# Kernel optimization log

Hardware: AMD Instinct MI355X
Metric: run time of the kernel (lower is better)

## Reference

```python
import jax, jax.numpy as jnp
import numpy as np

N, D, H, E = 50000, 64, 8, 800000
NEG_SLOPE = 0.2


def setup_inputs() -> dict:
    key = jax.random.key(0)
    k1, k2, k3 = jax.random.split(key, 3)
    h_t = jax.random.normal(k1, (N, D), dtype=jnp.float32)
    edge_index = jax.random.randint(k2, (2, E), 0, N, dtype=jnp.int64)
    # xavier-uniform-like init for att [H, 2D]
    limit = float(np.sqrt(6.0 / (H + 2 * D)))
    att = jax.random.uniform(k3, (H, 2 * D), dtype=jnp.float32, minval=-limit, maxval=limit)
    return {"h_t": h_t, "edge_index": edge_index, "att": att}


def reference(h_t, edge_index, att):
    src, dst = edge_index[0], edge_index[1]
    # att[:, :D] multiplies h_i (dst features), att[:, D:] multiplies h_j (src features)
    # einsum('ehd,hd->eh', cat([h_i, h_j]), att) == (h_t @ att_dst.T)[dst] + (h_t @ att_src.T)[src]
    s_dst = h_t @ att[:, :D].T   # [N, H]
    s_src = h_t @ att[:, D:].T   # [N, H]
    e = s_dst[dst] + s_src[src]  # [E, H]
    e = jnp.where(e >= 0, e, NEG_SLOPE * e)  # leaky_relu
    # segment softmax over dst groups (numerically stable)
    e_max = jax.ops.segment_max(e, dst, num_segments=N)          # [N, H]
    ex = jnp.exp(e - e_max[dst])                                  # [E, H]
    denom = jax.ops.segment_sum(ex, dst, num_segments=N)         # [N, H]
    alpha = ex / denom[dst]                                       # [E, H]
    # weighted messages and scatter-add aggregate
    m = h_t[src][:, None, :] * alpha[:, :, None]                  # [E, H, D]
    out = jax.ops.segment_sum(m, dst, num_segments=N)             # [N, H, D]
    out = jnp.where(out > 0, out, jnp.expm1(out))                 # elu
    return out.reshape(N, H * D)
```

## Files before the change

### kernel.cpp

```cpp
#include <hip/hip_runtime.h>
#include <math.h>

#define NN 50000
#define DD 64
#define HH 8
#define EE 800000
#define NEG_SLOPE 0.2f
#define WPB 4
#define SCAN_B 1024
#define NB1 ((NN + SCAN_B - 1) / SCAN_B)

__global__ __launch_bounds__(256) void scores_kernel(
    const float* __restrict__ h_t, const float* __restrict__ att,
    float* __restrict__ s_dst, float* __restrict__ s_src) {
  __shared__ float hs[32 * 66];
  __shared__ float att_s[8 * 130];
  int tid = threadIdx.x;
  int node0 = blockIdx.x * 32;
  for (int q = tid; q < HH * 2 * DD; q += 256) {
    int h = q >> 7, k = q & 127;
    att_s[h * 130 + k] = att[q];
  }
  for (int q = tid; q < 32 * DD; q += 256) {
    int nl = q >> 6, d = q & 63;
    hs[nl * 66 + d] = (node0 + nl < NN) ? h_t[(size_t)(node0 + nl) * DD + d] : 0.0f;
  }
  __syncthreads();
  int nl = tid >> 3, h = tid & 7;
  int n = node0 + nl;
  float accd = 0.f, accs = 0.f;
#pragma unroll
  for (int d = 0; d < DD; ++d) {
    float hv = hs[nl * 66 + d];
    accd += hv * att_s[h * 130 + d];
    accs += hv * att_s[h * 130 + DD + d];
  }
  if (n < NN) {
    s_dst[n * HH + h] = accd;
    s_src[n * HH + h] = accs;
  }
}

__global__ __launch_bounds__(256) void count_kernel(const int* __restrict__ ei,
                                                    int* __restrict__ counts,
                                                    int* __restrict__ rank) {
  int t = blockIdx.x * 256 + threadIdx.x;
  if (t >= EE / 4) return;
  int4 v = ((const int4*)(ei + EE))[t];
  int4 r;
  r.x = atomicAdd(&counts[v.x], 1);
  r.y = atomicAdd(&counts[v.y], 1);
  r.z = atomicAdd(&counts[v.z], 1);
  r.w = atomicAdd(&counts[v.w], 1);
  ((int4*)rank)[t] = r;
}

__global__ __launch_bounds__(256) void scan1_kernel(const int* __restrict__ counts,
                                                    int* __restrict__ bsum) {
  int t = threadIdx.x;
  int base = blockIdx.x * SCAN_B + t * 4;
  int s = 0;
  if (base + 3 < NN) {
    int4 v = *(const int4*)(counts + base);
    s = v.x + v.y + v.z + v.w;
  } else {
    for (int k = 0; k < 4; ++k)
      if (base + k < NN) s += counts[base + k];
  }
#pragma unroll
  for (int m = 1; m < 64; m <<= 1) s += __shfl_xor(s, m);
  __shared__ int wsum[4];
  if ((t & 63) == 0) wsum[t >> 6] = s;
  __syncthreads();
  if (t == 0) bsum[blockIdx.x] = wsum[0] + wsum[1] + wsum[2] + wsum[3];
}

__global__ void scan2_kernel(const int* __restrict__ bsum, int* __restrict__ boff,
                             int* __restrict__ row_start) {
  int lane = threadIdx.x;
  int v = (lane < NB1) ? bsum[lane] : 0;
  int incl = v;
#pragma unroll
  for (int off = 1; off < 64; off <<= 1) {
    int u = __shfl_up(incl, off);
    if (lane >= off) incl += u;
  }
  if (lane < NB1) boff[lane] = incl - v;
  if (lane == 0) row_start[NN] = EE;
}

__global__ __launch_bounds__(256) void scan3_kernel(const int* __restrict__ counts,
                                                    const int* __restrict__ boff,
                                                    int* __restrict__ row_start) {
  int t = threadIdx.x, lane = t & 63, w = t >> 6;
  int base = blockIdx.x * SCAN_B + t * 4;
  int c[4] = {0, 0, 0, 0};
  bool full = (base + 3 < NN);
  if (full) {
    int4 v = *(const int4*)(counts + base);
    c[0] = v.x; c[1] = v.y; c[2] = v.z; c[3] = v.w;
  } else {
    for (int k = 0; k < 4; ++k)
      if (base + k < NN) c[k] = counts[base + k];
  }
  int tot = c[0] + c[1] + c[2] + c[3];
  int incl = tot;
#pragma unroll
  for (int off = 1; off < 64; off <<= 1) {
    int u = __shfl_up(incl, off);
    if (lane >= off) incl += u;
  }
  __shared__ int wt[4];
  if (lane == 63) wt[w] = incl;
  __syncthreads();
  int wpre = 0;
  for (int q = 0; q < w; ++q) wpre += wt[q];
  int p = boff[blockIdx.x] + wpre + incl - tot;
  int o0 = p, o1 = p + c[0], o2 = o1 + c[1], o3 = o2 + c[2];
  if (full) {
    *(int4*)(row_start + base) = make_int4(o0, o1, o2, o3);
  } else {
    int o[4] = {o0, o1, o2, o3};
    for (int k = 0; k < 4; ++k)
      if (base + k < NN) row_start[base + k] = o[k];
  }
}

__global__ __launch_bounds__(256) void fill_kernel(
    const int* __restrict__ ei, const int* __restrict__ row_start,
    const int* __restrict__ rank, int* __restrict__ sorted_src) {
  int t = blockIdx.x * 256 + threadIdx.x;
  if (t >= EE / 4) return;
  int4 s = ((const int4*)ei)[t];
  int4 d = ((const int4*)(ei + EE))[t];
  int4 r = ((const int4*)rank)[t];
  sorted_src[row_start[d.x] + r.x] = s.x;
  sorted_src[row_start[d.y] + r.y] = s.y;
  sorted_src[row_start[d.z] + r.z] = s.z;
  sorted_src[row_start[d.w] + r.w] = s.w;
}

__global__ __launch_bounds__(256) void fused_kernel(
    const float* __restrict__ h_t, const float* __restrict__ s_dst,
    const float* __restrict__ s_src, const int* __restrict__ row_start,
    const int* __restrict__ sorted_src, float* __restrict__ out) {
  __shared__ float p_lds[WPB][64][8];
  __shared__ int src_lds[WPB][64];
  int w = threadIdx.x >> 6, lane = threadIdx.x & 63;
  int n = blockIdx.x * WPB + w;
  if (n >= NN) return;
  float (*pw)[8] = p_lds[w];
  int* sw = src_lds[w];
  int beg = row_start[n], end = row_start[n + 1];
  int deg = end - beg;
  size_t ob = (size_t)n * 512 + lane;
  if (deg == 0) {
#pragma unroll
    for (int h = 0; h < 8; ++h) out[ob + h * 64] = 0.f;
    return;
  }
  int i = lane >> 3, hh = lane & 7;
  float sd = s_dst[n * 8 + hh];
  float m = -INFINITY, sum = 0.f;
  float acc[8];
#pragma unroll
  for (int h = 0; h < 8; ++h) acc[h] = 0.f;

  if (deg <= 64) {
    float v[8];
    int sreg[8];
#pragma unroll
    for (int k = 0; k < 8; ++k) {
      int e = i + 8 * k;
      if (e < deg) {
        int s = sorted_src[beg + e];
        sreg[k] = s;
        float x = sd + s_src[s * 8 + hh];
        x = x >= 0.f ? x : NEG_SLOPE * x;
        v[k] = x;
        m = fmaxf(m, x);
      }
    }
#pragma unroll
    for (int msk = 8; msk < 64; msk <<= 1) m = fmaxf(m, __shfl_xor(m, msk));
#pragma unroll
    for (int k = 0; k < 8; ++k) {
      int e = i + 8 * k;
      if (e < deg) {
        float p = __expf(v[k] - m);
        sum += p;
        pw[e][hh] = p;
        if (hh == 0) sw[e] = sreg[k];
      }
    }
#pragma unroll
    for (int msk = 8; msk < 64; msk <<= 1) sum += __shfl_xor(sum, msk);
    __builtin_amdgcn_wave_barrier();
    for (int e = 0; e < deg; ++e) {
      int s = sw[e];
      float hv = h_t[(size_t)s * 64 + lane];
      float4 pa = *(const float4*)&pw[e][0];
      float4 pb = *(const float4*)&pw[e][4];
      acc[0] = fmaf(hv, pa.x, acc[0]);
      acc[1] = fmaf(hv, pa.y, acc[1]);
      acc[2] = fmaf(hv, pa.z, acc[2]);
      acc[3] = fmaf(hv, pa.w, acc[3]);
      acc[4] = fmaf(hv, pb.x, acc[4]);
      acc[5] = fmaf(hv, pb.y, acc[5]);
      acc[6] = fmaf(hv, pb.z, acc[6]);
      acc[7] = fmaf(hv, pb.w, acc[7]);
    }
  } else {
    for (int c = 0; c < deg; c += 64) {
      int cnt = min(64, deg - c);
#pragma unroll
      for (int k = 0; k < 8; ++k) {
        int le = i + 8 * k;
        if (le < cnt) {
          int s = sorted_src[beg + c + le];
          float x = sd + s_src[s * 8 + hh];
          x = x >= 0.f ? x : NEG_SLOPE * x;
          m = fmaxf(m, x);
        }
      }
    }
#pragma unroll
    for (int msk = 8; msk < 64; msk <<= 1) m = fmaxf(m, __shfl_xor(m, msk));
    for (int c = 0; c < deg; c += 64) {
      int cnt = min(64, deg - c);
      __builtin_amdgcn_wave_barrier();
#pragma unroll
      for (int k = 0; k < 8; ++k) {
        int le = i + 8 * k;
        if (le < cnt) {
          int s = sorted_src[beg + c + le];
          float x = sd + s_src[s * 8 + hh];
          x = x >= 0.f ? x : NEG_SLOPE * x;
          float p = __expf(x - m);
          sum += p;
          pw[le][hh] = p;
          if (hh == 0) sw[le] = s;
        }
      }
      __builtin_amdgcn_wave_barrier();
      for (int e = 0; e < cnt; ++e) {
        int s = sw[e];
        float hv = h_t[(size_t)s * 64 + lane];
        float4 pa = *(const float4*)&pw[e][0];
        float4 pb = *(const float4*)&pw[e][4];
        acc[0] = fmaf(hv, pa.x, acc[0]);
        acc[1] = fmaf(hv, pa.y, acc[1]);
        acc[2] = fmaf(hv, pa.z, acc[2]);
        acc[3] = fmaf(hv, pa.w, acc[3]);
        acc[4] = fmaf(hv, pb.x, acc[4]);
        acc[5] = fmaf(hv, pb.y, acc[5]);
        acc[6] = fmaf(hv, pb.z, acc[6]);
        acc[7] = fmaf(hv, pb.w, acc[7]);
      }
    }
#pragma unroll
    for (int msk = 8; msk < 64; msk <<= 1) sum += __shfl_xor(sum, msk);
  }
  float rdv = 1.0f / sum;
#pragma unroll
  for (int h = 0; h < 8; ++h) {
    float rd = __shfl(rdv, h);
    float r = acc[h] * rd;
    r = r > 0.f ? r : expm1f(r);
    out[ob + h * 64] = r;
  }
}

extern "C" void kernel_launch(void* const* d_in, const int* in_sizes, int n_in,
                              void* d_out, int out_size, void* d_ws, size_t ws_size,
                              hipStream_t stream) {
  const float* h_t = (const float*)d_in[0];
  const int* ei = (const int*)d_in[1];
  const float* att = (const float*)d_in[2];
  float* out = (float*)d_out;

  char* ws = (char*)d_ws;
  size_t off = 0;
  auto alloc = [&](size_t bytes) {
    size_t cur = off;
    off += (bytes + 255) & ~(size_t)255;
    return cur;
  };
  float* s_dst = (float*)(ws + alloc((size_t)NN * HH * 4));
  float* s_src = (float*)(ws + alloc((size_t)NN * HH * 4));
  size_t zero_off = off;
  int* counts = (int*)(ws + alloc((size_t)NN * 4));
  size_t zero_bytes = off - zero_off;
  int* row_start = (int*)(ws + alloc((size_t)(NN + 1) * 4));
  int* sorted_src = (int*)(ws + alloc((size_t)EE * 4));
  int* rank = (int*)(ws + alloc((size_t)EE * 4));
  int* bsum = (int*)(ws + alloc((size_t)NB1 * 4));
  int* boff = (int*)(ws + alloc((size_t)NB1 * 4));

  hipMemsetAsync(ws + zero_off, 0, zero_bytes, stream);
  scores_kernel<<<(NN + 31) / 32, 256, 0, stream>>>(h_t, att, s_dst, s_src);
  count_kernel<<<(EE / 4 + 255) / 256, 256, 0, stream>>>(ei, counts, rank);
  scan1_kernel<<<NB1, 256, 0, stream>>>(counts, bsum);
  scan2_kernel<<<1, 64, 0, stream>>>(bsum, boff, row_start);
  scan3_kernel<<<NB1, 256, 0, stream>>>(counts, boff, row_start);
  fill_kernel<<<(EE / 4 + 255) / 256, 256, 0, stream>>>(ei, row_start, rank,
                                                        sorted_src);
  fused_kernel<<<NN / WPB, 256, 0, stream>>>(h_t, s_dst, s_src, row_start,
                                             sorted_src, out);
}
```

Baseline: 262.2 us.

## Gather bf16 node features in fused aggregation and merge scores with count kernel

Writes a bf16 copy of h_t inside the score kernel and has the aggregation loop gather 2 bf16 features per lane, with each half-wave handling alternate edges, then combines the halves by shuffle. This halves the gather bytes per edge and lets the final store be float2-wide. The separate score and count kernels become one launch split by block index, and the two degree branches are unified into one chunked loop. bf16 rounding of messages adds precision error against the fp32 reference.

```diff
diff --git a/kernel.cpp b/kernel.cpp
--- a/kernel.cpp
+++ b/kernel.cpp
@@ -9,21 +9,54 @@
 #define WPB 4
 #define SCAN_B 1024
 #define NB1 ((NN + SCAN_B - 1) / SCAN_B)
-
-__global__ __launch_bounds__(256) void scores_kernel(
+#define NB_SC ((NN + 31) / 32)
+#define NB_CT ((EE / 4 + 255) / 256)
+
+#define FMA16(H0, H1, PA, PB)                                              \
+  acc[0] = fmaf(H0, PA.x, acc[0]);   acc[1] = fmaf(H1, PA.x, acc[1]);      \
+  acc[2] = fmaf(H0, PA.y, acc[2]);   acc[3] = fmaf(H1, PA.y, acc[3]);      \
+  acc[4] = fmaf(H0, PA.z, acc[4]);   acc[5] = fmaf(H1, PA.z, acc[5]);      \
+  acc[6] = fmaf(H0, PA.w, acc[6]);   acc[7] = fmaf(H1, PA.w, acc[7]);      \
+  acc[8] = fmaf(H0, PB.x, acc[8]);   acc[9] = fmaf(H1, PB.x, acc[9]);      \
+  acc[10] = fmaf(H0, PB.y, acc[10]); acc[11] = fmaf(H1, PB.y, acc[11]);    \
+  acc[12] = fmaf(H0, PB.z, acc[12]); acc[13] = fmaf(H1, PB.z, acc[13]);    \
+  acc[14] = fmaf(H0, PB.w, acc[14]); acc[15] = fmaf(H1, PB.w, acc[15]);
+
+__global__ __launch_bounds__(256) void combo_kernel(
     const float* __restrict__ h_t, const float* __restrict__ att,
-    float* __restrict__ s_dst, float* __restrict__ s_src) {
+    const int* __restrict__ ei, float* __restrict__ s_dst,
+    float* __restrict__ s_src, unsigned short* __restrict__ h_bf,
+    int* __restrict__ counts, int* __restrict__ rank) {
+  if (blockIdx.x >= NB_SC) {
+    int t = (blockIdx.x - NB_SC) * 256 + threadIdx.x;
+    if (t >= EE / 4) return;
+    int4 v = ((const int4*)(ei + EE))[t];
+    int4 r;
+    r.x = atomicAdd(&counts[v.x], 1);
+    r.y = atomicAdd(&counts[v.y], 1);
+    r.z = atomicAdd(&counts[v.z], 1);
+    r.w = atomicAdd(&counts[v.w], 1);
+    ((int4*)rank)[t] = r;
+    return;
+  }
   __shared__ float hs[32 * 66];
   __shared__ float att_s[8 * 130];
   int tid = threadIdx.x;
   int node0 = blockIdx.x * 32;
   for (int q = tid; q < HH * 2 * DD; q += 256) {
-    int h = q >> 7, k = q & 127;
-    att_s[h * 130 + k] = att[q];
+    att_s[(q >> 7) * 130 + (q & 127)] = att[q];
   }
   for (int q = tid; q < 32 * DD; q += 256) {
     int nl = q >> 6, d = q & 63;
-    hs[nl * 66 + d] = (node0 + nl < NN) ? h_t[(size_t)(node0 + nl) * DD + d] : 0.0f;
+    int nd = node0 + nl;
+    float val = 0.f;
+    if (nd < NN) {
+      val = h_t[(size_t)nd * 64 + d];
+      unsigned u = __float_as_uint(val);
+      unsigned r = (u + 0x7fffu + ((u >> 16) & 1u)) >> 16;
+      h_bf[(size_t)nd * 64 + d] = (unsigned short)r;
+    }
+    hs[nl * 66 + d] = val;
   }
   __syncthreads();
   int nl = tid >> 3, h = tid & 7;
@@ -36,23 +69,9 @@
     accs += hv * att_s[h * 130 + DD + d];
   }
   if (n < NN) {
-    s_dst[n * HH + h] = accd;
-    s_src[n * HH + h] = accs;
-  }
-}
-
-__global__ __launch_bounds__(256) void count_kernel(const int* __restrict__ ei,
-                                                    int* __restrict__ counts,
-                                                    int* __restrict__ rank) {
-  int t = blockIdx.x * 256 + threadIdx.x;
-  if (t >= EE / 4) return;
-  int4 v = ((const int4*)(ei + EE))[t];
-  int4 r;
-  r.x = atomicAdd(&counts[v.x], 1);
-  r.y = atomicAdd(&counts[v.y], 1);
-  r.z = atomicAdd(&counts[v.z], 1);
-  r.w = atomicAdd(&counts[v.w], 1);
-  ((int4*)rank)[t] = r;
+    s_dst[n * 8 + h] = accd;
+    s_src[n * 8 + h] = accs;
+  }
 }
 
 __global__ __launch_bounds__(256) void scan1_kernel(const int* __restrict__ counts,
@@ -141,133 +160,135 @@
 }
 
 __global__ __launch_bounds__(256) void fused_kernel(
-    const float* __restrict__ h_t, const float* __restrict__ s_dst,
+    const unsigned short* __restrict__ h_bf, const float* __restrict__ s_dst,
     const float* __restrict__ s_src, const int* __restrict__ row_start,
     const int* __restrict__ sorted_src, float* __restrict__ out) {
   __shared__ float p_lds[WPB][64][8];
   __shared__ int src_lds[WPB][64];
   int w = threadIdx.x >> 6, lane = threadIdx.x & 63;
   int n = blockIdx.x * WPB + w;
-  if (n >= NN) return;
   float (*pw)[8] = p_lds[w];
   int* sw = src_lds[w];
   int beg = row_start[n], end = row_start[n + 1];
   int deg = end - beg;
-  size_t ob = (size_t)n * 512 + lane;
+  int p2 = lane & 31, half = lane >> 5;
+  float* outn = out + (size_t)n * 512;
   if (deg == 0) {
 #pragma unroll
-    for (int h = 0; h < 8; ++h) out[ob + h * 64] = 0.f;
+    for (int h4 = 0; h4 < 4; ++h4) {
+      int h = half * 4 + h4;
+      *(float2*)(outn + h * 64 + 2 * p2) = make_float2(0.f, 0.f);
+    }
     return;
   }
   int i = lane >> 3, hh = lane & 7;
   float sd = s_dst[n * 8 + hh];
   float m = -INFINITY, sum = 0.f;
-  float acc[8];
-#pragma unroll
-  for (int h = 0; h < 8; ++h) acc[h] = 0.f;
-
-  if (deg <= 64) {
-    float v[8];
-    int sreg[8];
+  float acc[16];
+#pragma unroll
+  for (int q = 0; q < 16; ++q) acc[q] = 0.f;
+  float v[8];
+  int sreg[8];
+  bool stash = (deg <= 64);
+
+  for (int c = 0; c < deg; c += 64) {
+    int cnt = min(64, deg - c);
 #pragma unroll
     for (int k = 0; k < 8; ++k) {
-      int e = i + 8 * k;
-      if (e < deg) {
-        int s = sorted_src[beg + e];
-        sreg[k] = s;
+      int le = i + 8 * k;
+      if (le < cnt) {
+        int s = sorted_src[beg + c + le];
         float x = sd + s_src[s * 8 + hh];
         x = x >= 0.f ? x : NEG_SLOPE * x;
-        v[k] = x;
+        if (stash) { v[k] = x; sreg[k] = s; }
         m = fmaxf(m, x);
       }
     }
-#pragma unroll
-    for (int msk = 8; msk < 64; msk <<= 1) m = fmaxf(m, __shfl_xor(m, msk));
+  }
+#pragma unroll
+  for (int msk = 8; msk < 64; msk <<= 1) m = fmaxf(m, __shfl_xor(m, msk));
+
+  for (int c = 0; c < deg; c += 64) {
+    int cnt = min(64, deg - c);
+    int sfirst = 0;
 #pragma unroll
     for (int k = 0; k < 8; ++k) {
-      int e = i + 8 * k;
-      if (e < deg) {
-        float p = __expf(v[k] - m);
-        sum += p;
-        pw[e][hh] = p;
-        if (hh == 0) sw[e] = sreg[k];
+      int le = i + 8 * k;
+      if (le < cnt) {
+        int s;
+        float x;
+        if (stash) {
+          s = sreg[k];
+          x = v[k];
+        } else {
+          s = sorted_src[beg + c + le];
+          x = sd + s_src[s * 8 + hh];
+          x = x >= 0.f ? x : NEG_SLOPE * x;
+        }
+        float pv = __expf(x - m);
+        sum += pv;
+        pw[le][hh] = pv;
+        if (hh == 0) sw[le] = s;
+        if (le == 0) sfirst = s;
       }
     }
-#pragma unroll
-    for (int msk = 8; msk < 64; msk <<= 1) sum += __shfl_xor(sum, msk);
+    int cnt2 = cnt;
+    if (cnt & 1) {
+      if (lane < 8) pw[cnt][lane] = 0.f;
+      if (lane == 0) sw[cnt] = sfirst;
+      cnt2 = cnt + 1;
+    }
     __builtin_amdgcn_wave_barrier();
-    for (int e = 0; e < deg; ++e) {
-      int s = sw[e];
-      float hv = h_t[(size_t)s * 64 + lane];
-      float4 pa = *(const float4*)&pw[e][0];
-      float4 pb = *(const float4*)&pw[e][4];
-      acc[0] = fmaf(hv, pa.x, acc[0]);
-      acc[1] = fmaf(hv, pa.y, acc[1]);
-      acc[2] = fmaf(hv, pa.z, acc[2]);
-      acc[3] = fmaf(hv, pa.w, acc[3]);
-      acc[4] = fmaf(hv, pb.x, acc[4]);
-      acc[5] = fmaf(hv, pb.y, acc[5]);
-      acc[6] = fmaf(hv, pb.z, acc[6]);
-      acc[7] = fmaf(hv, pb.w, acc[7]);
-    }
-  } else {
-    for (int c = 0; c < deg; c += 64) {
-      int cnt = min(64, deg - c);
-#pragma unroll
-      for (int k = 0; k < 8; ++k) {
-        int le = i + 8 * k;
-        if (le < cnt) {
-          int s = sorted_src[beg + c + le];
-          float x = sd + s_src[s * 8 + hh];
-          x = x >= 0.f ? x : NEG_SLOPE * x;
-          m = fmaxf(m, x);
-        }
-      }
-    }
-#pragma unroll
-    for (int msk = 8; msk < 64; msk <<= 1) m = fmaxf(m, __shfl_xor(m, msk));
-    for (int c = 0; c < deg; c += 64) {
-      int cnt = min(64, deg - c);
-      __builtin_amdgcn_wave_barrier();
-#pragma unroll
-      for (int k = 0; k < 8; ++k) {
-        int le = i + 8 * k;
-        if (le < cnt) {
-          int s = sorted_src[beg + c + le];
-          float x = sd + s_src[s * 8 + hh];
-          x = x >= 0.f ? x : NEG_SLOPE * x;
-          float p = __expf(x - m);
-          sum += p;
-          pw[le][hh] = p;
-          if (hh == 0) sw[le] = s;
-        }
-      }
-      __builtin_amdgcn_wave_barrier();
-      for (int e = 0; e < cnt; ++e) {
-        int s = sw[e];
-        float hv = h_t[(size_t)s * 64 + lane];
-        float4 pa = *(const float4*)&pw[e][0];
-        float4 pb = *(const float4*)&pw[e][4];
-        acc[0] = fmaf(hv, pa.x, acc[0]);
-        acc[1] = fmaf(hv, pa.y, acc[1]);
-        acc[2] = fmaf(hv, pa.z, acc[2]);
-        acc[3] = fmaf(hv, pa.w, acc[3]);
-        acc[4] = fmaf(hv, pb.x, acc[4]);
-        acc[5] = fmaf(hv, pb.y, acc[5]);
-        acc[6] = fmaf(hv, pb.z, acc[6]);
-        acc[7] = fmaf(hv, pb.w, acc[7]);
-      }
-    }
-#pragma unroll
-    for (int msk = 8; msk < 64; msk <<= 1) sum += __shfl_xor(sum, msk);
-  }
+    int e = 0;
+    for (; e + 4 <= cnt2; e += 4) {
+      int eA = e + half, eB = e + 2 + half;
+      int s0 = sw[eA], s1 = sw[eB];
+      unsigned u0 = *(const unsigned*)(h_bf + (size_t)s0 * 64 + 2 * p2);
+      unsigned u1 = *(const unsigned*)(h_bf + (size_t)s1 * 64 + 2 * p2);
+      float4 pa0 = *(const float4*)&pw[eA][0];
+      float4 pb0 = *(const float4*)&pw[eA][4];
+      float4 pa1 = *(const float4*)&pw[eB][0];
+      float4 pb1 = *(const float4*)&pw[eB][4];
+      float a0 = __uint_as_float(u0 << 16);
+      float a1 = __uint_as_float(u0 & 0xffff0000u);
+      FMA16(a0, a1, pa0, pb0);
+      float b0 = __uint_as_float(u1 << 16);
+      float b1 = __uint_as_float(u1 & 0xffff0000u);
+      FMA16(b0, b1, pa1, pb1);
+    }
+    for (; e < cnt2; e += 2) {
+      int eA = e + half;
+      int s0 = sw[eA];
+      unsigned u0 = *(const unsigned*)(h_bf + (size_t)s0 * 64 + 2 * p2);
+      float4 pa0 = *(const float4*)&pw[eA][0];
+      float4 pb0 = *(const float4*)&pw[eA][4];
+      float a0 = __uint_as_float(u0 << 16);
+      float a1 = __uint_as_float(u0 & 0xffff0000u);
+      FMA16(a0, a1, pa0, pb0);
+    }
+    __builtin_amdgcn_wave_barrier();
+  }
+#pragma unroll
+  for (int msk = 8; msk < 64; msk <<= 1) sum += __shfl_xor(sum, msk);
+#pragma unroll
+  for (int q = 0; q < 16; ++q) acc[q] += __shfl_xor(acc[q], 32);
+
   float rdv = 1.0f / sum;
 #pragma unroll
-  for (int h = 0; h < 8; ++h) {
+  for (int h4 = 0; h4 < 4; ++h4) {
+    int h = half * 4 + h4;
     float rd = __shfl(rdv, h);
-    float r = acc[h] * rd;
-    r = r > 0.f ? r : expm1f(r);
-    out[ob + h * 64] = r;
+    float r0, r1;
+    if (half == 0) {
+      r0 = acc[2 * h4] * rd;
+      r1 = acc[2 * h4 + 1] * rd;
+    } else {
+      r0 = acc[8 + 2 * h4] * rd;
+      r1 = acc[9 + 2 * h4] * rd;
+    }
+    r0 = r0 > 0.f ? r0 : expm1f(r0);
+    r1 = r1 > 0.f ? r1 : expm1f(r1);
+    *(float2*)(outn + h * 64 + 2 * p2) = make_float2(r0, r1);
   }
 }
 
@@ -288,6 +309,7 @@
   };
   float* s_dst = (float*)(ws + alloc((size_t)NN * HH * 4));
   float* s_src = (float*)(ws + alloc((size_t)NN * HH * 4));
+  unsigned short* h_bf = (unsigned short*)(ws + alloc((size_t)NN * DD * 2));
   size_t zero_off = off;
   int* counts = (int*)(ws + alloc((size_t)NN * 4));
   size_t zero_bytes = off - zero_off;
@@ -298,13 +320,13 @@
   int* boff = (int*)(ws + alloc((size_t)NB1 * 4));
 
   hipMemsetAsync(ws + zero_off, 0, zero_bytes, stream);
-  scores_kernel<<<(NN + 31) / 32, 256, 0, stream>>>(h_t, att, s_dst, s_src);
-  count_kernel<<<(EE / 4 + 255) / 256, 256, 0, stream>>>(ei, counts, rank);
+  combo_kernel<<<NB_SC + NB_CT, 256, 0, stream>>>(h_t, att, ei, s_dst, s_src,
+                                                  h_bf, counts, rank);
   scan1_kernel<<<NB1, 256, 0, stream>>>(counts, bsum);
   scan2_kernel<<<1, 64, 0, stream>>>(bsum, boff, row_start);
   scan3_kernel<<<NB1, 256, 0, stream>>>(counts, boff, row_start);
   fill_kernel<<<(EE / 4 + 255) / 256, 256, 0, stream>>>(ei, row_start, rank,
                                                         sorted_src);
-  fused_kernel<<<NN / WPB, 256, 0, stream>>>(h_t, s_dst, s_src, row_start,
+  fused_kernel<<<NN / WPB, 256, 0, stream>>>(h_bf, s_dst, s_src, row_start,
                                              sorted_src, out);
 }
```

After: 266.5 us. No clear change (+1.6%).
